# Optimization experiments

Hardware: AMD Instinct MI355X
Metric: run time of the kernel (lower is better)

## Reference

```python
import jax, jax.numpy as jnp
import numpy as np

HEADS = 8
NEG_SLOPE = 0.2


def _leaky(x):
    return jnp.where(x >= 0, x, NEG_SLOPE * x)


def _layernorm(x, g, b):
    # torch nn.LayerNorm over last dim, eps=1e-5, biased variance
    m = x.mean(-1, keepdims=True)
    v = ((x - m) ** 2).mean(-1, keepdims=True)
    return (x - m) / jnp.sqrt(v + 1e-5) * g + b


def _batchnorm(x, g, b):
    # training-mode BatchNorm2d, eps=1e-4, biased variance over (N,H,W)
    m = x.mean((0, 2, 3), keepdims=True)
    v = ((x - m) ** 2).mean((0, 2, 3), keepdims=True)
    return (x - m) / jnp.sqrt(v + 1e-4) * g[None, :, None, None] + b[None, :, None, None]


def _depthwise3x3(x, k):
    # x: (B,C,H,W), k: (C,1,3,3) depthwise kernel
    C = x.shape[1]
    return jax.lax.conv_general_dilated(
        x, k, (1, 1), 'SAME', feature_group_count=C,
        dimension_numbers=('NCHW', 'OIHW', 'NCHW'))


def _attn_layer(x, wq, wk, wv, wproj, bproj, wpos):
    # x: (B,H,W,C) channels-last; MDTA-style transposed attention
    b, H, W, C = x.shape
    d = C // HEADS
    xf = x.reshape(b, H * W, C)
    q, k, v = xf @ wq, xf @ wk, xf @ wv  # (b, n, C)

    def split(t):
        return t.reshape(b, H * W, HEADS, d).transpose(0, 2, 3, 1)  # (b, h, d, n)

    qh, kh, vh = split(q), split(k), split(v)
    # F.normalize over token axis n (eps=1e-12)
    qn = qh / jnp.maximum(jnp.sqrt((qh * qh).sum(-1, keepdims=True)), 1e-12)
    kn = kh / jnp.maximum(jnp.sqrt((kh * kh).sum(-1, keepdims=True)), 1e-12)
    attn = jax.nn.softmax(jnp.einsum('bhdn,bhen->bhde', kn, qn), axis=-1)  # (b,h,d,d)
    o = jnp.einsum('bhde,bhen->bhdn', attn, vh)  # (b,h,d,n)
    o = o.transpose(0, 3, 1, 2).reshape(b, H * W, C)
    out_c = (o @ wproj + bproj).reshape(b, H, W, C)
    out_p = _depthwise3x3(v.reshape(b, H, W, C).transpose(0, 3, 1, 2), wpos).transpose(0, 2, 3, 1)
    return out_c * out_p


def _transformer_block(x, wq, wk, wv, wproj, bproj, wpos, ln_g, ln_b, wff):
    # x: NCHW -> BHWC, 2 (attn + prenorm-FF) residual blocks, -> NCHW
    x = x.transpose(0, 2, 3, 1)
    for i in range(wq.shape[0]):
        x = _attn_layer(x, wq[i], wk[i], wv[i], wproj[i], bproj[i], wpos[i]) + x
        x = _layernorm(x, ln_g[i], ln_b[i]) @ wff[i] + x
    return x.transpose(0, 3, 1, 2)


def _saa(x, w1, w2):
    # SAA_Block: 8x8 spatial pool, global min-max norm, bmm correlation, SE gating
    b, c, H, W = x.shape
    y = x.reshape(b, c, 8, H // 8, 8, W // 8).mean((3, 5)).reshape(b, c, 64)
    y = (y - y.min()) / (y.max() - y.min())
    y = jnp.einsum('bci,bdi->bcd', y, y).mean(2)[:, :, None, None]  # (b,c,1,1)
    g = (x * y).mean((2, 3))  # (b,c) global avg pool
    g = jax.nn.sigmoid(_leaky(g @ w1) @ w2)
    return x * g[:, :, None, None]


def setup_inputs() -> dict:
    key = jax.random.key(0)
    B, C, H, W = 16, 64, 128, 128
    L = 2  # num_blocks in Transformer_block
    ks = jax.random.split(key, 12)
    s = 0.05
    inp = {
        'x': jax.random.normal(ks[0], (B, C, H, W), jnp.float32),
        'wq': jax.random.normal(ks[1], (L, C, C), jnp.float32) * s,
        'wk': jax.random.normal(ks[2], (L, C, C), jnp.float32) * s,
        'wv': jax.random.normal(ks[3], (L, C, C), jnp.float32) * s,
        'wproj': jax.random.normal(ks[4], (L, C, C), jnp.float32) * s,
        'bproj': jnp.zeros((L, C), jnp.float32),
        'wpos': jax.random.normal(ks[5], (L, C, 1, 3, 3), jnp.float32) * s,
        'ln_g': jnp.ones((L, C), jnp.float32),
        'ln_b': jnp.zeros((L, C), jnp.float32),
        'wff': jax.random.normal(ks[6], (L, C, C), jnp.float32) * s,
        'bn1_g': jnp.ones((C,), jnp.float32),
        'bn1_b': jnp.zeros((C,), jnp.float32),
        'wd': jax.random.normal(ks[7], (C, C), jnp.float32) * s,
        'bn2_g': jnp.ones((C,), jnp.float32),
        'bn2_b': jnp.zeros((C,), jnp.float32),
        'saa_w1': jax.random.normal(ks[8], (C, C // 16), jnp.float32) * s,
        'saa_w2': jax.random.normal(ks[9], (C // 16, C), jnp.float32) * s,
    }
    return inp


def reference(x, wq, wk, wv, wproj, bproj, wpos, ln_g, ln_b, wff,
              bn1_g, bn1_b, wd, bn2_g, bn2_b, saa_w1, saa_w2):
    # res path: C (Transformer_block) -> L -> B -> D (1x1 conv) -> L -> B
    r = _transformer_block(x, wq, wk, wv, wproj, bproj, wpos, ln_g, ln_b, wff)
    r = _batchnorm(_leaky(r), bn1_g, bn1_b)
    r = jnp.einsum('bchw,co->bohw', r, wd)  # 1x1 conv, bias=False
    r = _batchnorm(_leaky(r), bn2_g, bn2_b)
    return _saa(r + x, saa_w1, saa_w2)
```

## Files before the change

kernel.cpp:

```cpp
#include <hip/hip_runtime.h>

constexpr int NB = 16, NC = 64, NH = 128, NW = 128;
constexpr int NPIX = NH * NW;
constexpr int NTOT = NB * NPIX;
constexpr size_t BUF = (size_t)NTOT * NC;

constexpr size_t OFF_A   = 0;
constexpr size_t OFF_ACT = BUF;
constexpr size_t OFF_V   = 2 * BUF;
constexpr size_t OFF_S   = 3 * BUF;
constexpr size_t OFF_QSQ = OFF_S   + 2*16*512;
constexpr size_t OFF_KSQ = OFF_QSQ + 2048;
constexpr size_t OFF_BN1 = OFF_KSQ + 2048;
constexpr size_t OFF_BN2 = OFF_BN1 + 128;
constexpr size_t ZERO_FLOATS = 16384 + 2048 + 2048 + 128 + 128;
constexpr size_t OFF_W2  = OFF_BN2 + 128;
constexpr size_t OFF_AB1 = OFF_W2  + 131072;
constexpr size_t OFF_AB2 = OFF_AB1 + 128;
constexpr size_t OFF_Y   = OFF_AB2 + 128;
constexpr size_t OFF_GATE= OFF_Y   + 65536;

__device__ __forceinline__ float leaky(float x) { return x >= 0.f ? x : 0.2f * x; }
#define RFL __builtin_amdgcn_readfirstlane
#define WAVES_EU(mn, mx) __attribute__((amdgpu_waves_per_eu(mn, mx)))

__global__ __launch_bounds__(256) void k_transpose_in(const float* __restrict__ x,
                                                      float* __restrict__ A) {
  __shared__ float t[64][65];
  int blk = blockIdx.x;
  int b = blk >> 8;
  int p0 = (blk & 255) * 64;
  int tid = threadIdx.x;
  int cq = tid >> 6, p = tid & 63;
  for (int i = 0; i < 16; i++) {
    int c = cq * 16 + i;
    t[p][c] = x[((size_t)(b * 64 + c)) * NPIX + p0 + p];
  }
  __syncthreads();
  int pq = tid >> 6, c = tid & 63;
  for (int i = 0; i < 16; i++) {
    int p2 = pq * 16 + i;
    A[((size_t)(b * NPIX + p0 + p2)) * 64 + c] = t[p2][c];
  }
}

__global__ __launch_bounds__(256) WAVES_EU(2, 2) void k_qk(
    const float* __restrict__ act,
    const float* __restrict__ wq, const float* __restrict__ wk,
    float* __restrict__ S, float* __restrict__ qsq, float* __restrict__ ksq,
    int l) {
  __shared__ float xb[8][64];
  int tid = threadIdx.x;
  int lane = tid & 63;
  int bid = blockIdx.x;
  int sbid = (bid & 7) * 128 + (bid >> 3);
  int wid = RFL((int)(sbid * 4 + (tid >> 6)));
  int wslot = (tid >> 6) & 3;
  int b = wid >> 8;
  const float* Wq = wq + (size_t)l * 4096;
  const float* Wk = wk + (size_t)l * 4096;
  float wqc[64], wkc[64];
#pragma unroll
  for (int ci = 0; ci < 64; ci++) {
    wqc[ci] = Wq[ci * 64 + lane];
    wkc[ci] = Wk[ci * 64 + lane];
  }
  float Sacc[8];
#pragma unroll
  for (int e = 0; e < 8; e++) Sacc[e] = 0.f;
  float qsa = 0.f, ksa = 0.f;
  int gbase = lane & 56;
  int base = wid * 4096;
  float xl = act[base + lane];
#pragma unroll 1
  for (int p = 0; p < 64; p++) {
    int off = base + p * 64;
    int xs = wslot * 2 + (p & 1);
    xb[xs][lane] = xl;
    float xn = 0.f;
    if (p < 63) xn = act[off + 64 + lane];
    const float4* x4p = (const float4*)xb[xs];
    float q = 0.f, k = 0.f;
#pragma unroll
    for (int i = 0; i < 16; i++) {
      float4 x4 = x4p[i];
      q = fmaf(x4.x, wqc[4*i+0], q);
      k = fmaf(x4.x, wkc[4*i+0], k);
      q = fmaf(x4.y, wqc[4*i+1], q);
      k = fmaf(x4.y, wkc[4*i+1], k);
      q = fmaf(x4.z, wqc[4*i+2], q);
      k = fmaf(x4.z, wkc[4*i+2], k);
      q = fmaf(x4.w, wqc[4*i+3], q);
      k = fmaf(x4.w, wkc[4*i+3], k);
    }
    qsa = fmaf(q, q, qsa);
    ksa = fmaf(k, k, ksa);
#pragma unroll
    for (int e = 0; e < 8; e++) {
      float qe = __shfl(q, gbase + e, 64);
      Sacc[e] = fmaf(k, qe, Sacc[e]);
    }
    xl = xn;
  }
  float* Sb = S + ((size_t)l * 16 + b) * 512 + lane * 8;
#pragma unroll
  for (int e = 0; e < 8; e++) atomicAdd(Sb + e, Sacc[e]);
  atomicAdd(qsq + ((size_t)l * 16 + b) * 64 + lane, qsa);
  atomicAdd(ksq + ((size_t)l * 16 + b) * 64 + lane, ksa);
}

__global__ __launch_bounds__(256) WAVES_EU(4, 4) void k_mat_v(
    const float* __restrict__ act, const float* __restrict__ wv,
    float* __restrict__ v, int l) {
  __shared__ float xb[8][64];
  int tid = threadIdx.x;
  int lane = tid & 63;
  int bid = blockIdx.x;
  int sbid = (bid & 7) * 128 + (bid >> 3);
  int wid = RFL((int)(sbid * 4 + (tid >> 6)));
  int wslot = (tid >> 6) & 3;
  const float* Wv = wv + (size_t)l * 4096;
  float wvc[64];
#pragma unroll
  for (int ci = 0; ci < 64; ci++) wvc[ci] = Wv[ci * 64 + lane];
  int base = wid * 4096;
  float xl = act[base + lane];
#pragma unroll 1
  for (int p = 0; p < 64; p++) {
    int off = base + p * 64;
    int xs = wslot * 2 + (p & 1);
    xb[xs][lane] = xl;
    float xn = 0.f;
    if (p < 63) xn = act[off + 64 + lane];
    const float4* x4p = (const float4*)xb[xs];
    float a0 = 0.f, a1 = 0.f, a2 = 0.f, a3 = 0.f;
#pragma unroll
    for (int i = 0; i < 16; i++) {
      float4 x4 = x4p[i];
      a0 = fmaf(x4.x, wvc[4*i+0], a0);
      a1 = fmaf(x4.y, wvc[4*i+1], a1);
      a2 = fmaf(x4.z, wvc[4*i+2], a2);
      a3 = fmaf(x4.w, wvc[4*i+3], a3);
    }
    v[off + lane] = (a0 + a1) + (a2 + a3);
    xl = xn;
  }
}

__global__ __launch_bounds__(64) void k_attn(const float* __restrict__ S,
    const float* __restrict__ qsq, const float* __restrict__ ksq,
    const float* __restrict__ wproj, float* __restrict__ W2, int l) {
  int b = blockIdx.x, t = threadIdx.x;
  __shared__ float A[8][8][8];
  const float* Sb = S + ((size_t)l * 16 + b) * 512;
  const float* qs = qsq + ((size_t)l * 16 + b) * 64;
  const float* ks = ksq + ((size_t)l * 16 + b) * 64;
  int h = t >> 3, d = t & 7;
  float kden = fmaxf(sqrtf(ks[h * 8 + d]), 1e-12f);
  float pre[8];
  float mx = -1e30f;
#pragma unroll
  for (int e = 0; e < 8; e++) {
    float qden = fmaxf(sqrtf(qs[h * 8 + e]), 1e-12f);
    pre[e] = Sb[(h * 8 + d) * 8 + e] / (kden * qden);
    mx = fmaxf(mx, pre[e]);
  }
  float sum = 0.f;
#pragma unroll
  for (int e = 0; e < 8; e++) { pre[e] = expf(pre[e] - mx); sum += pre[e]; }
  float inv = 1.f / sum;
#pragma unroll
  for (int e = 0; e < 8; e++) A[h][d][e] = pre[e] * inv;
  __syncthreads();
  int co = t;
  const float* wp = wproj + (size_t)l * 4096;
  float* W2b = W2 + ((size_t)l * 16 + b) * 4096;
#pragma unroll 1
  for (int cin = 0; cin < 64; cin++) {
    int hh2 = cin >> 3, e = cin & 7;
    float acc = 0.f;
#pragma unroll
    for (int dd = 0; dd < 8; dd++)
      acc = fmaf(A[hh2][dd][e], wp[(hh2 * 8 + dd) * 64 + co], acc);
    W2b[cin * 64 + co] = acc;
  }
}

__global__ __launch_bounds__(256) WAVES_EU(2, 2) void k_attnout_ff(
    const float* __restrict__ vbuf, const float* __restrict__ actin,
    float* __restrict__ actout, const float* __restrict__ W2all,
    const float* __restrict__ bproj, const float* __restrict__ wpos,
    const float* __restrict__ lng, const float* __restrict__ lnb,
    const float* __restrict__ wff, float* __restrict__ bn1, int l, int dobn) {
  __shared__ float xb[8][64], yb[8][64];
  int tid = threadIdx.x;
  int lane = tid & 63;
  int bid = blockIdx.x;
  int sbid = (bid & 7) * 128 + (bid >> 3);
  int wid = RFL((int)(sbid * 4 + (tid >> 6)));
  int wslot = (tid >> 6) & 3;
  int b = wid >> 8;
  int widb = wid & 255;
  int hh = widb >> 1;
  int c0 = (widb & 1) * 64;
  const float* W2 = W2all + ((size_t)l * 16 + b) * 4096;
  const float* WF = wff + (size_t)l * 4096;
  float w2c[64], wfc[64];
#pragma unroll
  for (int ci = 0; ci < 64; ci++) {
    w2c[ci] = W2[ci * 64 + lane];
    wfc[ci] = WF[ci * 64 + lane];
  }
  float wpc[9];
#pragma unroll
  for (int kk = 0; kk < 9; kk++) wpc[kk] = wpos[(size_t)l * 576 + lane * 9 + kk];
  float bp = bproj[l * 64 + lane];
  float G  = lng[l * 64 + lane];
  float Bb = lnb[l * 64 + lane];

  bool okm = (hh > 0), okp = (hh < 127);
  int base = wid * 4096;
  float Lm = 0.f, L0 = 0.f, Lp = 0.f, Cm = 0.f, C0, Cp = 0.f;
  C0 = vbuf[base + lane];
  if (okm) Cm = vbuf[base - 8192 + lane];
  if (okp) Cp = vbuf[base + 8192 + lane];
  if (c0 == 64) {
    L0 = vbuf[base - 64 + lane];
    if (okm) Lm = vbuf[base - 64 - 8192 + lane];
    if (okp) Lp = vbuf[base - 64 + 8192 + lane];
  }
  float av = actin[base + lane];
  float s_bn = 0.f, s2_bn = 0.f;
#pragma unroll 1
  for (int p = 0; p < 64; p++) {
    int off = base + p * 64;
    float Rm = 0.f, R0 = 0.f, Rp = 0.f, avn = 0.f;
    bool okc = (c0 + p + 1 < 128);
    if (okc) {
      R0 = vbuf[off + 64 + lane];
      if (okm) Rm = vbuf[off + 64 - 8192 + lane];
      if (okp) Rp = vbuf[off + 64 + 8192 + lane];
    }
    if (p < 63) avn = actin[off + 64 + lane];
    int xs = wslot * 2 + (p & 1);
    xb[xs][lane] = C0;
    const float4* x4p = (const float4*)xb[xs];
    float a0 = 0.f, a1 = 0.f, a2 = 0.f, a3 = 0.f;
#pragma unroll
    for (int i = 0; i < 16; i++) {
      float4 x4 = x4p[i];
      a0 = fmaf(x4.x, w2c[4*i+0], a0);
      a1 = fmaf(x4.y, w2c[4*i+1], a1);
      a2 = fmaf(x4.z, w2c[4*i+2], a2);
      a3 = fmaf(x4.w, w2c[4*i+3], a3);
    }
    float acc = (a0 + a1) + (a2 + a3) + bp;
    float op = Lm * wpc[0] + Cm * wpc[1] + Rm * wpc[2]
             + L0 * wpc[3] + C0 * wpc[4] + R0 * wpc[5]
             + Lp * wpc[6] + Cp * wpc[7] + Rp * wpc[8];
    float y = acc * op + av;
    float t1 = y, t2 = y * y;
#pragma unroll
    for (int m = 1; m < 64; m <<= 1) {
      t1 += __shfl_xor(t1, m, 64);
      t2 += __shfl_xor(t2, m, 64);
    }
    float mean = t1 * (1.f / 64.f);
    float var = t2 * (1.f / 64.f) - mean * mean;
    float iv = 1.f / sqrtf(var + 1e-5f);
    float yn = (y - mean) * iv * G + Bb;
    yb[xs][lane] = yn;
    const float4* y4p = (const float4*)yb[xs];
    float o0 = 0.f, o1 = 0.f, o2 = 0.f, o3 = 0.f;
#pragma unroll
    for (int i = 0; i < 16; i++) {
      float4 y4 = y4p[i];
      o0 = fmaf(y4.x, wfc[4*i+0], o0);
      o1 = fmaf(y4.y, wfc[4*i+1], o1);
      o2 = fmaf(y4.z, wfc[4*i+2], o2);
      o3 = fmaf(y4.w, wfc[4*i+3], o3);
    }
    float out = y + (o0 + o1) + (o2 + o3);
    if (dobn) {
      float lo = leaky(out);
      s_bn += lo;
      s2_bn = fmaf(lo, lo, s2_bn);
    }
    actout[off + lane] = out;
    Lm = Cm; L0 = C0; Lp = Cp;
    Cm = Rm; C0 = R0; Cp = Rp;
    av = avn;
  }
  if (dobn) {
    atomicAdd(&bn1[lane], s_bn);
    atomicAdd(&bn1[64 + lane], s2_bn);
  }
}

__global__ __launch_bounds__(64) void k_bnfin(const float* __restrict__ sums,
                                              const float* __restrict__ g,
                                              const float* __restrict__ bt,
                                              float* __restrict__ ab, float eps) {
  int c = threadIdx.x;
  float m = sums[c] * (1.f / (float)NTOT);
  float v = sums[64 + c] * (1.f / (float)NTOT) - m * m;
  float a = g[c] / sqrtf(v + eps);
  ab[c] = a;
  ab[64 + c] = bt[c] - m * a;
}

__global__ __launch_bounds__(256) WAVES_EU(4, 4) void k_conv1x1(
    const float* __restrict__ act,
    const float* __restrict__ ab, const float* __restrict__ wd,
    float* __restrict__ outv, float* __restrict__ bn2) {
  __shared__ float xb[8][64];
  int tid = threadIdx.x;
  int lane = tid & 63;
  int bid = blockIdx.x;
  int sbid = (bid & 7) * 128 + (bid >> 3);
  int wid = RFL((int)(sbid * 4 + (tid >> 6)));
  int wslot = (tid >> 6) & 3;
  float wdc[64];
#pragma unroll
  for (int ci = 0; ci < 64; ci++) wdc[ci] = wd[ci * 64 + lane];
  float a1l = ab[lane], b1l = ab[64 + lane];
  float s_bn = 0.f, s2_bn = 0.f;
  int base = wid * 4096;
  float xl = act[base + lane];
#pragma unroll 1
  for (int p = 0; p < 64; p++) {
    int off = base + p * 64;
    float tl = fmaf(a1l, leaky(xl), b1l);
    int xs = wslot * 2 + (p & 1);
    xb[xs][lane] = tl;
    float xn = 0.f;
    if (p < 63) xn = act[off + 64 + lane];
    const float4* x4p = (const float4*)xb[xs];
    float a0 = 0.f, a1 = 0.f, a2 = 0.f, a3 = 0.f;
#pragma unroll
    for (int i = 0; i < 16; i++) {
      float4 x4 = x4p[i];
      a0 = fmaf(x4.x, wdc[4*i+0], a0);
      a1 = fmaf(x4.y, wdc[4*i+1], a1);
      a2 = fmaf(x4.z, wdc[4*i+2], a2);
      a3 = fmaf(x4.w, wdc[4*i+3], a3);
    }
    float out = leaky((a0 + a1) + (a2 + a3));
    s_bn += out;
    s2_bn = fmaf(out, out, s2_bn);
    outv[off + lane] = out;
    xl = xn;
  }
  atomicAdd(&bn2[lane], s_bn);
  atomicAdd(&bn2[64 + lane], s2_bn);
}

__global__ __launch_bounds__(512) void k_pool(const float* __restrict__ lr2,
    const float* __restrict__ xA, const float* __restrict__ ab2,
    float* __restrict__ y) {
  int blk = blockIdx.x;
  int b = blk >> 4;
  int br = (blk >> 1) & 7;
  int half = blk & 1;
  int t = threadIdx.x;
  int c = t & 63;
  int w8 = t >> 6;
  float a2 = ab2[c], b2 = ab2[64 + c];
  float acc[4];
#pragma unroll
  for (int i = 0; i < 4; i++) acc[i] = 0.f;
#pragma unroll 1
  for (int r = 0; r < 16; r++) {
    size_t base = ((size_t)(b * NPIX + (br * 16 + r) * NW + half * 64)) * 64;
#pragma unroll
    for (int i = 0; i < 8; i++) {
      size_t idx = base + (size_t)i * 512 + t;
      float sv = fmaf(a2, lr2[idx], b2) + xA[idx];
      acc[i >> 1] += sv;
    }
  }
  __shared__ float red[8][4][64];
#pragma unroll
  for (int i = 0; i < 4; i++) red[w8][i][c] = acc[i];
  __syncthreads();
  if (t < 256) {
    int bin = t >> 6, c2 = t & 63;
    float s = 0.f;
#pragma unroll
    for (int w = 0; w < 8; w++) s += red[w][bin][c2];
    y[((size_t)(b * 64 + c2)) * 64 + br * 8 + half * 4 + bin] = s * (1.f / 256.f);
  }
}

__global__ __launch_bounds__(1024) void k_saa(const float* __restrict__ y,
    const float* __restrict__ w1, const float* __restrict__ w2,
    float* __restrict__ gate) {
  int t = threadIdx.x;
  __shared__ float rmin[1024], rmax[1024];
  float mn = 1e30f, mx = -1e30f;
#pragma unroll 1
  for (int i = 0; i < 64; i++) {
    float vv = y[(size_t)i * 1024 + t];
    mn = fminf(mn, vv);
    mx = fmaxf(mx, vv);
  }
  rmin[t] = mn; rmax[t] = mx;
  __syncthreads();
  for (int s = 512; s > 0; s >>= 1) {
    if (t < s) {
      rmin[t] = fminf(rmin[t], rmin[t + s]);
      rmax[t] = fmaxf(rmax[t], rmax[t + s]);
    }
    __syncthreads();
  }
  float gmn = rmin[0], gmx = rmax[0];
  float inv = 1.f / (gmx - gmn);
  __syncthreads();
  int b = t >> 6;
  int i6 = t & 63;
  __shared__ float tl[16][64];
  {
    const float* yb2 = y + (size_t)b * 4096;
    float s = 0.f;
#pragma unroll 1
    for (int cl = 0; cl < 64; cl++) s += yb2[cl * 64 + i6];
    tl[b][i6] = (s - 64.f * gmn) * inv;
  }
  __syncthreads();
  int cc = i6;
  const float* yc = y + (size_t)b * 4096 + cc * 64;
  float z = 0.f, ms = 0.f;
#pragma unroll 1
  for (int ii = 0; ii < 64; ii++) {
    float yr = yc[ii];
    z = fmaf((yr - gmn) * inv, tl[b][ii], z);
    ms += yr;
  }
  z *= (1.f / 64.f);
  ms *= (1.f / 64.f);
  __shared__ float g0l[16][64];
  g0l[b][cc] = z * ms;
  __syncthreads();
  __shared__ float hl[16][4];
  if (t < 64) {
    int bb = t >> 2, j = t & 3;
    float h = 0.f;
#pragma unroll 1
    for (int c2 = 0; c2 < 64; c2++) h = fmaf(g0l[bb][c2], w1[c2 * 4 + j], h);
    hl[bb][j] = leaky(h);
  }
  __syncthreads();
  float acc = 0.f;
#pragma unroll
  for (int j = 0; j < 4; j++) acc = fmaf(hl[b][j], w2[j * 64 + cc], acc);
  gate[t] = 1.f / (1.f + expf(-acc));
}

__global__ __launch_bounds__(256) void k_out(const float* __restrict__ lr2,
    const float* __restrict__ xA, const float* __restrict__ ab2,
    const float* __restrict__ gate, float* __restrict__ out) {
  __shared__ float tile[64][65];
  int blk = blockIdx.x;
  int b = blk >> 8;
  int p0 = (blk & 255) * 64;
  int tid = threadIdx.x;
  int c = tid & 63, pq = tid >> 6;
  float a2 = ab2[c], b2 = ab2[64 + c];
  for (int i = 0; i < 16; i++) {
    int p = pq * 16 + i;
    size_t idx = ((size_t)(b * NPIX + p0 + p)) * 64 + c;
    tile[p][c] = fmaf(a2, lr2[idx], b2) + xA[idx];
  }
  __syncthreads();
  int p = tid & 63, cq = tid >> 6;
  for (int i = 0; i < 16; i++) {
    int c2 = cq * 16 + i;
    out[((size_t)(b * 64 + c2)) * NPIX + p0 + p] = tile[p][c2] * gate[b * 64 + c2];
  }
}

extern "C" void kernel_launch(void* const* d_in, const int* in_sizes, int n_in,
                              void* d_out, int out_size, void* d_ws, size_t ws_size,
                              hipStream_t stream) {
  const float* x     = (const float*)d_in[0];
  const float* wq    = (const float*)d_in[1];
  const float* wk    = (const float*)d_in[2];
  const float* wv    = (const float*)d_in[3];
  const float* wproj = (const float*)d_in[4];
  const float* bproj = (const float*)d_in[5];
  const float* wpos  = (const float*)d_in[6];
  const float* ln_g  = (const float*)d_in[7];
  const float* ln_b  = (const float*)d_in[8];
  const float* wff   = (const float*)d_in[9];
  const float* bn1_g = (const float*)d_in[10];
  const float* bn1_b = (const float*)d_in[11];
  const float* wd    = (const float*)d_in[12];
  const float* bn2_g = (const float*)d_in[13];
  const float* bn2_b = (const float*)d_in[14];
  const float* sw1   = (const float*)d_in[15];
  const float* sw2   = (const float*)d_in[16];

  float* ws   = (float*)d_ws;
  float* A    = ws + OFF_A;
  float* ACT  = ws + OFF_ACT;
  float* V    = ws + OFF_V;
  float* S    = ws + OFF_S;
  float* QSQ  = ws + OFF_QSQ;
  float* KSQ  = ws + OFF_KSQ;
  float* BN1S = ws + OFF_BN1;
  float* BN2S = ws + OFF_BN2;
  float* W2   = ws + OFF_W2;
  float* AB1  = ws + OFF_AB1;
  float* AB2  = ws + OFF_AB2;
  float* Y    = ws + OFF_Y;
  float* GATE = ws + OFF_GATE;

  hipMemsetAsync((void*)S, 0, ZERO_FLOATS * sizeof(float), stream);

  k_transpose_in<<<4096, 256, 0, stream>>>(x, A);

  for (int l = 0; l < 2; l++) {
    const float* in = (l == 0) ? A : ACT;
    k_qk<<<1024, 256, 0, stream>>>(in, wq, wk, S, QSQ, KSQ, l);
    k_mat_v<<<1024, 256, 0, stream>>>(in, wv, V, l);
    k_attn<<<16, 64, 0, stream>>>(S, QSQ, KSQ, wproj, W2, l);
    k_attnout_ff<<<1024, 256, 0, stream>>>(V, in, ACT, W2, bproj, wpos,
                                           ln_g, ln_b, wff, BN1S, l, l == 1);
  }

  k_bnfin<<<1, 64, 0, stream>>>(BN1S, bn1_g, bn1_b, AB1, 1e-4f);
  k_conv1x1<<<1024, 256, 0, stream>>>(ACT, AB1, wd, V, BN2S);
  k_bnfin<<<1, 64, 0, stream>>>(BN2S, bn2_g, bn2_b, AB2, 1e-4f);
  k_pool<<<256, 512, 0, stream>>>(V, A, AB2, Y);
  k_saa<<<1, 1024, 0, stream>>>(Y, sw1, sw2, GATE);
  k_out<<<4096, 256, 0, stream>>>(V, A, AB2, GATE, (float*)d_out);
}
```

Before: 1.331 ms.

## Replace Q/K projection with Gram matrix of activations and fuse pooling into producers

Removes the separate Q/K projection pass. A per-batch Gram matrix X^T X is accumulated in the same pass that computes V. A small per-batch kernel then derives the Q·K scores and the token norms algebraically as Wk^T G Wq, diag(Wq^T G Wq) and diag(Wk^T G Wk). The 8x8 spatial pooling is folded into the V/gram kernel (for the input) and the 1x1 conv kernel (for the residual-path output) as partial sums written with atomics. This replaces the full pooling read pass with a tiny finalize kernel, and the affine BN2 is applied to the pooled means. In exchange it adds 64 extra accumulator registers per lane, more atomics and an LDS reduction. Forming the Gram matrix in float32 may also change rounding slightly.

After: 1.714 ms. +28.7%, slower.

```diff
diff --git a/kernel.cpp b/kernel.cpp
--- a/kernel.cpp
+++ b/kernel.cpp
@@ -8,13 +8,13 @@
 constexpr size_t OFF_A   = 0;
 constexpr size_t OFF_ACT = BUF;
 constexpr size_t OFF_V   = 2 * BUF;
-constexpr size_t OFF_S   = 3 * BUF;
-constexpr size_t OFF_QSQ = OFF_S   + 2*16*512;
-constexpr size_t OFF_KSQ = OFF_QSQ + 2048;
-constexpr size_t OFF_BN1 = OFF_KSQ + 2048;
+constexpr size_t OFF_G   = 3 * BUF;
+constexpr size_t OFF_BN1 = OFF_G   + 131072;
 constexpr size_t OFF_BN2 = OFF_BN1 + 128;
-constexpr size_t ZERO_FLOATS = 16384 + 2048 + 2048 + 128 + 128;
-constexpr size_t OFF_W2  = OFF_BN2 + 128;
+constexpr size_t OFF_PXA = OFF_BN2 + 128;
+constexpr size_t OFF_PLR = OFF_PXA + 65536;
+constexpr size_t ZERO_FLOATS = 131072 + 128 + 128 + 65536 + 65536;
+constexpr size_t OFF_W2  = OFF_PLR + 65536;
 constexpr size_t OFF_AB1 = OFF_W2  + 131072;
 constexpr size_t OFF_AB2 = OFF_AB1 + 128;
 constexpr size_t OFF_Y   = OFF_AB2 + 128;
@@ -23,6 +23,7 @@
 __device__ __forceinline__ float leaky(float x) { return x >= 0.f ? x : 0.2f * x; }
 #define RFL __builtin_amdgcn_readfirstlane
 #define WAVES_EU(mn, mx) __attribute__((amdgpu_waves_per_eu(mn, mx)))
+#define PIN(x) asm volatile("" : "+v"(x))
 
 __global__ __launch_bounds__(256) void k_transpose_in(const float* __restrict__ x,
                                                       float* __restrict__ A) {
@@ -44,91 +45,38 @@
   }
 }
 
-__global__ __launch_bounds__(256) WAVES_EU(2, 2) void k_qk(
-    const float* __restrict__ act,
-    const float* __restrict__ wq, const float* __restrict__ wk,
-    float* __restrict__ S, float* __restrict__ qsq, float* __restrict__ ksq,
-    int l) {
+__global__ __launch_bounds__(256) WAVES_EU(2, 2) void k_gramv(
+    const float* __restrict__ act, const float* __restrict__ wv,
+    float* __restrict__ v, float* __restrict__ G, float* __restrict__ Pxa,
+    int l, int dopool) {
   __shared__ float xb[8][64];
+  __shared__ float Gred[2][64][65];
   int tid = threadIdx.x;
   int lane = tid & 63;
+  int w = tid >> 6;
   int bid = blockIdx.x;
   int sbid = (bid & 7) * 128 + (bid >> 3);
-  int wid = RFL((int)(sbid * 4 + (tid >> 6)));
-  int wslot = (tid >> 6) & 3;
+  int wid = RFL((int)(sbid * 4 + w));
   int b = wid >> 8;
-  const float* Wq = wq + (size_t)l * 4096;
-  const float* Wk = wk + (size_t)l * 4096;
-  float wqc[64], wkc[64];
-#pragma unroll
-  for (int ci = 0; ci < 64; ci++) {
-    wqc[ci] = Wq[ci * 64 + lane];
-    wkc[ci] = Wk[ci * 64 + lane];
-  }
-  float Sacc[8];
-#pragma unroll
-  for (int e = 0; e < 8; e++) Sacc[e] = 0.f;
-  float qsa = 0.f, ksa = 0.f;
-  int gbase = lane & 56;
+  int widb = wid & 255;
+  int hh = widb >> 1;
+  int c0 = (widb & 1) * 64;
+  const float* Wv = wv + (size_t)l * 4096;
+  float wvc[64];
+#pragma unroll
+  for (int ci = 0; ci < 64; ci++) wvc[ci] = Wv[ci * 64 + lane];
+#pragma unroll
+  for (int ci = 0; ci < 64; ci++) PIN(wvc[ci]);
+  float Gacc[64];
+#pragma unroll
+  for (int e = 0; e < 64; e++) Gacc[e] = 0.f;
+  float xp0 = 0.f, xp1 = 0.f, xp2 = 0.f, xp3 = 0.f, run = 0.f;
   int base = wid * 4096;
   float xl = act[base + lane];
 #pragma unroll 1
   for (int p = 0; p < 64; p++) {
     int off = base + p * 64;
-    int xs = wslot * 2 + (p & 1);
-    xb[xs][lane] = xl;
-    float xn = 0.f;
-    if (p < 63) xn = act[off + 64 + lane];
-    const float4* x4p = (const float4*)xb[xs];
-    float q = 0.f, k = 0.f;
-#pragma unroll
-    for (int i = 0; i < 16; i++) {
-      float4 x4 = x4p[i];
-      q = fmaf(x4.x, wqc[4*i+0], q);
-      k = fmaf(x4.x, wkc[4*i+0], k);
-      q = fmaf(x4.y, wqc[4*i+1], q);
-      k = fmaf(x4.y, wkc[4*i+1], k);
-      q = fmaf(x4.z, wqc[4*i+2], q);
-      k = fmaf(x4.z, wkc[4*i+2], k);
-      q = fmaf(x4.w, wqc[4*i+3], q);
-      k = fmaf(x4.w, wkc[4*i+3], k);
-    }
-    qsa = fmaf(q, q, qsa);
-    ksa = fmaf(k, k, ksa);
-#pragma unroll
-    for (int e = 0; e < 8; e++) {
-      float qe = __shfl(q, gbase + e, 64);
-      Sacc[e] = fmaf(k, qe, Sacc[e]);
-    }
-    xl = xn;
-  }
-  float* Sb = S + ((size_t)l * 16 + b) * 512 + lane * 8;
-#pragma unroll
-  for (int e = 0; e < 8; e++) atomicAdd(Sb + e, Sacc[e]);
-  atomicAdd(qsq + ((size_t)l * 16 + b) * 64 + lane, qsa);
-  atomicAdd(ksq + ((size_t)l * 16 + b) * 64 + lane, ksa);
-}
-
-__global__ __launch_bounds__(256) WAVES_EU(4, 4) void k_mat_v(
-    const float* __restrict__ act, const float* __restrict__ wv,
-    float* __restrict__ v, int l) {
-  __shared__ float xb[8][64];
-  int tid = threadIdx.x;
-  int lane = tid & 63;
-  int bid = blockIdx.x;
-  int sbid = (bid & 7) * 128 + (bid >> 3);
-  int wid = RFL((int)(sbid * 4 + (tid >> 6)));
-  int wslot = (tid >> 6) & 3;
-  const float* Wv = wv + (size_t)l * 4096;
-  float wvc[64];
-#pragma unroll
-  for (int ci = 0; ci < 64; ci++) wvc[ci] = Wv[ci * 64 + lane];
-  int base = wid * 4096;
-  float xl = act[base + lane];
-#pragma unroll 1
-  for (int p = 0; p < 64; p++) {
-    int off = base + p * 64;
-    int xs = wslot * 2 + (p & 1);
+    int xs = w * 2 + (p & 1);
     xb[xs][lane] = xl;
     float xn = 0.f;
     if (p < 63) xn = act[off + 64 + lane];
@@ -138,50 +86,126 @@
     for (int i = 0; i < 16; i++) {
       float4 x4 = x4p[i];
       a0 = fmaf(x4.x, wvc[4*i+0], a0);
+      Gacc[4*i+0] = fmaf(x4.x, xl, Gacc[4*i+0]);
       a1 = fmaf(x4.y, wvc[4*i+1], a1);
+      Gacc[4*i+1] = fmaf(x4.y, xl, Gacc[4*i+1]);
       a2 = fmaf(x4.z, wvc[4*i+2], a2);
+      Gacc[4*i+2] = fmaf(x4.z, xl, Gacc[4*i+2]);
       a3 = fmaf(x4.w, wvc[4*i+3], a3);
+      Gacc[4*i+3] = fmaf(x4.w, xl, Gacc[4*i+3]);
     }
     v[off + lane] = (a0 + a1) + (a2 + a3);
+    run += xl;
+    if (p == 15) { xp0 = run; run = 0.f; }
+    if (p == 31) { xp1 = run; run = 0.f; }
+    if (p == 47) { xp2 = run; run = 0.f; }
+    if (p == 63) { xp3 = run; }
     xl = xn;
   }
-}
-
-__global__ __launch_bounds__(64) void k_attn(const float* __restrict__ S,
-    const float* __restrict__ qsq, const float* __restrict__ ksq,
+  __syncthreads();
+  if (w >= 2) {
+#pragma unroll
+    for (int e = 0; e < 64; e++) Gred[w - 2][lane][e] = Gacc[e];
+  }
+  __syncthreads();
+  if (w < 2) {
+#pragma unroll
+    for (int e = 0; e < 64; e++) Gacc[e] += Gred[w][lane][e];
+  }
+  __syncthreads();
+  if (w == 1) {
+#pragma unroll
+    for (int e = 0; e < 64; e++) Gred[0][lane][e] = Gacc[e];
+  }
+  __syncthreads();
+  if (w == 0) {
+    float* Gb = G + ((size_t)l * 16 + b) * 4096;
+#pragma unroll
+    for (int e = 0; e < 64; e++) {
+      float s = Gacc[e] + Gred[0][lane][e];
+      atomicAdd(Gb + lane * 64 + e, s);
+    }
+  }
+  if (dopool) {
+    int binbase = (hh >> 4) * 8 + (c0 >> 4);
+    float* P = Pxa + ((size_t)(b * 64 + lane)) * 64 + binbase;
+    atomicAdd(P + 0, xp0);
+    atomicAdd(P + 1, xp1);
+    atomicAdd(P + 2, xp2);
+    atomicAdd(P + 3, xp3);
+  }
+}
+
+__global__ __launch_bounds__(256) void k_attnW2(const float* __restrict__ G,
+    const float* __restrict__ wq, const float* __restrict__ wk,
     const float* __restrict__ wproj, float* __restrict__ W2, int l) {
+  __shared__ float Gl[64][65], Mq[64][65], Mk[64][65];
+  __shared__ float A[8][8][8];
+  __shared__ float qsql[64], ksql[64];
   int b = blockIdx.x, t = threadIdx.x;
-  __shared__ float A[8][8][8];
-  const float* Sb = S + ((size_t)l * 16 + b) * 512;
-  const float* qs = qsq + ((size_t)l * 16 + b) * 64;
-  const float* ks = ksq + ((size_t)l * 16 + b) * 64;
-  int h = t >> 3, d = t & 7;
-  float kden = fmaxf(sqrtf(ks[h * 8 + d]), 1e-12f);
-  float pre[8];
-  float mx = -1e30f;
-#pragma unroll
-  for (int e = 0; e < 8; e++) {
-    float qden = fmaxf(sqrtf(qs[h * 8 + e]), 1e-12f);
-    pre[e] = Sb[(h * 8 + d) * 8 + e] / (kden * qden);
-    mx = fmaxf(mx, pre[e]);
-  }
-  float sum = 0.f;
-#pragma unroll
-  for (int e = 0; e < 8; e++) { pre[e] = expf(pre[e] - mx); sum += pre[e]; }
-  float inv = 1.f / sum;
-#pragma unroll
-  for (int e = 0; e < 8; e++) A[h][d][e] = pre[e] * inv;
-  __syncthreads();
-  int co = t;
+  const float* Gg = G + ((size_t)l * 16 + b) * 4096;
+  for (int i = t; i < 4096; i += 256) Gl[i >> 6][i & 63] = Gg[i];
+  __syncthreads();
+  const float* Wq = wq + (size_t)l * 4096;
+  const float* Wk = wk + (size_t)l * 4096;
+  int j = t & 63, r0 = (t >> 6) * 16;
+#pragma unroll 1
+  for (int r = r0; r < r0 + 16; r++) {
+    float aq = 0.f, ak = 0.f;
+#pragma unroll
+    for (int c = 0; c < 64; c++) {
+      float g = Gl[r][c];
+      aq = fmaf(g, Wq[c * 64 + j], aq);
+      ak = fmaf(g, Wk[c * 64 + j], ak);
+    }
+    Mq[r][j] = aq;
+    Mk[r][j] = ak;
+  }
+  __syncthreads();
+  if (t < 64) {
+    float sq = 0.f, sk = 0.f;
+#pragma unroll
+    for (int r = 0; r < 64; r++) {
+      sq = fmaf(Wq[r * 64 + t], Mq[r][t], sq);
+      sk = fmaf(Wk[r * 64 + t], Mk[r][t], sk);
+    }
+    qsql[t] = sq;
+    ksql[t] = sk;
+  }
+  __syncthreads();
+  if (t < 64) {
+    int h = t >> 3;
+    float kden = fmaxf(sqrtf(ksql[t]), 1e-12f);
+    float pre[8];
+    float mx = -1e30f;
+#pragma unroll
+    for (int e = 0; e < 8; e++) {
+      int ef = h * 8 + e;
+      float s = 0.f;
+#pragma unroll
+      for (int r = 0; r < 64; r++) s = fmaf(Wk[r * 64 + t], Mq[r][ef], s);
+      float qden = fmaxf(sqrtf(qsql[ef]), 1e-12f);
+      pre[e] = s / (kden * qden);
+      mx = fmaxf(mx, pre[e]);
+    }
+    float sum = 0.f;
+#pragma unroll
+    for (int e = 0; e < 8; e++) { pre[e] = expf(pre[e] - mx); sum += pre[e]; }
+    float inv = 1.f / sum;
+#pragma unroll
+    for (int e = 0; e < 8; e++) A[h][t & 7][e] = pre[e] * inv;
+  }
+  __syncthreads();
   const float* wp = wproj + (size_t)l * 4096;
   float* W2b = W2 + ((size_t)l * 16 + b) * 4096;
-#pragma unroll 1
-  for (int cin = 0; cin < 64; cin++) {
-    int hh2 = cin >> 3, e = cin & 7;
+  int co = t & 63;
+#pragma unroll 1
+  for (int cin = r0; cin < r0 + 16; cin++) {
+    int h = cin >> 3, e = cin & 7;
     float acc = 0.f;
 #pragma unroll
     for (int dd = 0; dd < 8; dd++)
-      acc = fmaf(A[hh2][dd][e], wp[(hh2 * 8 + dd) * 64 + co], acc);
+      acc = fmaf(A[h][dd][e], wp[(h * 8 + dd) * 64 + co], acc);
     W2b[cin * 64 + co] = acc;
   }
 }
@@ -211,9 +235,13 @@
     w2c[ci] = W2[ci * 64 + lane];
     wfc[ci] = WF[ci * 64 + lane];
   }
+#pragma unroll
+  for (int ci = 0; ci < 64; ci++) { PIN(w2c[ci]); PIN(wfc[ci]); }
   float wpc[9];
 #pragma unroll
   for (int kk = 0; kk < 9; kk++) wpc[kk] = wpos[(size_t)l * 576 + lane * 9 + kk];
+#pragma unroll
+  for (int kk = 0; kk < 9; kk++) PIN(wpc[kk]);
   float bp = bproj[l * 64 + lane];
   float G  = lng[l * 64 + lane];
   float Bb = lnb[l * 64 + lane];
@@ -312,7 +340,8 @@
 __global__ __launch_bounds__(256) WAVES_EU(4, 4) void k_conv1x1(
     const float* __restrict__ act,
     const float* __restrict__ ab, const float* __restrict__ wd,
-    float* __restrict__ outv, float* __restrict__ bn2) {
+    float* __restrict__ outv, float* __restrict__ bn2,
+    float* __restrict__ Plr) {
   __shared__ float xb[8][64];
   int tid = threadIdx.x;
   int lane = tid & 63;
@@ -320,11 +349,18 @@
   int sbid = (bid & 7) * 128 + (bid >> 3);
   int wid = RFL((int)(sbid * 4 + (tid >> 6)));
   int wslot = (tid >> 6) & 3;
+  int b = wid >> 8;
+  int widb = wid & 255;
+  int hh = widb >> 1;
+  int c0 = (widb & 1) * 64;
   float wdc[64];
 #pragma unroll
   for (int ci = 0; ci < 64; ci++) wdc[ci] = wd[ci * 64 + lane];
+#pragma unroll
+  for (int ci = 0; ci < 64; ci++) PIN(wdc[ci]);
   float a1l = ab[lane], b1l = ab[64 + lane];
   float s_bn = 0.f, s2_bn = 0.f;
+  float xp0 = 0.f, xp1 = 0.f, xp2 = 0.f, xp3 = 0.f, run = 0.f;
   int base = wid * 4096;
   float xl = act[base + lane];
 #pragma unroll 1
@@ -349,47 +385,30 @@
     s_bn += out;
     s2_bn = fmaf(out, out, s2_bn);
     outv[off + lane] = out;
+    run += out;
+    if (p == 15) { xp0 = run; run = 0.f; }
+    if (p == 31) { xp1 = run; run = 0.f; }
+    if (p == 47) { xp2 = run; run = 0.f; }
+    if (p == 63) { xp3 = run; }
     xl = xn;
   }
   atomicAdd(&bn2[lane], s_bn);
   atomicAdd(&bn2[64 + lane], s2_bn);
-}
-
-__global__ __launch_bounds__(512) void k_pool(const float* __restrict__ lr2,
-    const float* __restrict__ xA, const float* __restrict__ ab2,
+  int binbase = (hh >> 4) * 8 + (c0 >> 4);
+  float* P = Plr + ((size_t)(b * 64 + lane)) * 64 + binbase;
+  atomicAdd(P + 0, xp0);
+  atomicAdd(P + 1, xp1);
+  atomicAdd(P + 2, xp2);
+  atomicAdd(P + 3, xp3);
+}
+
+__global__ __launch_bounds__(1024) void k_poolfin(const float* __restrict__ Plr,
+    const float* __restrict__ Pxa, const float* __restrict__ ab2,
     float* __restrict__ y) {
-  int blk = blockIdx.x;
-  int b = blk >> 4;
-  int br = (blk >> 1) & 7;
-  int half = blk & 1;
-  int t = threadIdx.x;
-  int c = t & 63;
-  int w8 = t >> 6;
-  float a2 = ab2[c], b2 = ab2[64 + c];
-  float acc[4];
-#pragma unroll
-  for (int i = 0; i < 4; i++) acc[i] = 0.f;
-#pragma unroll 1
-  for (int r = 0; r < 16; r++) {
-    size_t base = ((size_t)(b * NPIX + (br * 16 + r) * NW + half * 64)) * 64;
-#pragma unroll
-    for (int i = 0; i < 8; i++) {
-      size_t idx = base + (size_t)i * 512 + t;
-      float sv = fmaf(a2, lr2[idx], b2) + xA[idx];
-      acc[i >> 1] += sv;
-    }
-  }
-  __shared__ float red[8][4][64];
-#pragma unroll
-  for (int i = 0; i < 4; i++) red[w8][i][c] = acc[i];
-  __syncthreads();
-  if (t < 256) {
-    int bin = t >> 6, c2 = t & 63;
-    float s = 0.f;
-#pragma unroll
-    for (int w = 0; w < 8; w++) s += red[w][bin][c2];
-    y[((size_t)(b * 64 + c2)) * 64 + br * 8 + half * 4 + bin] = s * (1.f / 256.f);
-  }
+  int idx = blockIdx.x * 1024 + threadIdx.x;
+  int c = (idx >> 6) & 63;
+  y[idx] = fmaf(ab2[c], Plr[idx] * (1.f / 256.f), ab2[64 + c])
+         + Pxa[idx] * (1.f / 256.f);
 }
 
 __global__ __launch_bounds__(1024) void k_saa(const float* __restrict__ y,
@@ -504,34 +523,33 @@
   float* A    = ws + OFF_A;
   float* ACT  = ws + OFF_ACT;
   float* V    = ws + OFF_V;
-  float* S    = ws + OFF_S;
-  float* QSQ  = ws + OFF_QSQ;
-  float* KSQ  = ws + OFF_KSQ;
+  float* G    = ws + OFF_G;
   float* BN1S = ws + OFF_BN1;
   float* BN2S = ws + OFF_BN2;
+  float* PXA  = ws + OFF_PXA;
+  float* PLR  = ws + OFF_PLR;
   float* W2   = ws + OFF_W2;
   float* AB1  = ws + OFF_AB1;
   float* AB2  = ws + OFF_AB2;
   float* Y    = ws + OFF_Y;
   float* GATE = ws + OFF_GATE;
 
-  hipMemsetAsync((void*)S, 0, ZERO_FLOATS * sizeof(float), stream);
+  hipMemsetAsync((void*)G, 0, ZERO_FLOATS * sizeof(float), stream);
 
   k_transpose_in<<<4096, 256, 0, stream>>>(x, A);
 
   for (int l = 0; l < 2; l++) {
     const float* in = (l == 0) ? A : ACT;
-    k_qk<<<1024, 256, 0, stream>>>(in, wq, wk, S, QSQ, KSQ, l);
-    k_mat_v<<<1024, 256, 0, stream>>>(in, wv, V, l);
-    k_attn<<<16, 64, 0, stream>>>(S, QSQ, KSQ, wproj, W2, l);
+    k_gramv<<<1024, 256, 0, stream>>>(in, wv, V, G, PXA, l, l == 0);
+    k_attnW2<<<16, 256, 0, stream>>>(G, wq, wk, wproj, W2, l);
     k_attnout_ff<<<1024, 256, 0, stream>>>(V, in, ACT, W2, bproj, wpos,
                                            ln_g, ln_b, wff, BN1S, l, l == 1);
   }
 
   k_bnfin<<<1, 64, 0, stream>>>(BN1S, bn1_g, bn1_b, AB1, 1e-4f);
-  k_conv1x1<<<1024, 256, 0, stream>>>(ACT, AB1, wd, V, BN2S);
+  k_conv1x1<<<1024, 256, 0, stream>>>(ACT, AB1, wd, V, BN2S, PLR);
   k_bnfin<<<1, 64, 0, stream>>>(BN2S, bn2_g, bn2_b, AB2, 1e-4f);
-  k_pool<<<256, 512, 0, stream>>>(V, A, AB2, Y);
+  k_poolfin<<<64, 1024, 0, stream>>>(PLR, PXA, AB2, Y);
   k_saa<<<1, 1024, 0, stream>>>(Y, sw1, sw2, GATE);
   k_out<<<4096, 256, 0, stream>>>(V, A, AB2, GATE, (float*)d_out);
 }
```
